# Kernel optimization log

Hardware: AMD Instinct MI355X
Metric: run time of the kernel (lower is better)

The kernel has to match this reference:

```python
import jax, jax.numpy as jnp
import numpy as np

N_NODES = 50000
N_EDGES = 800000
D_IN = 128
D_OUT = 128


def setup_inputs() -> dict:
    key = jax.random.key(0)
    k1, k2, k3, k4, k5, k6 = jax.random.split(key, 6)
    x = jax.random.normal(k1, (N_NODES, D_IN), dtype=jnp.float32)
    weight = jax.random.normal(k2, (D_IN, D_OUT), dtype=jnp.float32)
    bias = jax.random.normal(k3, (D_OUT,), dtype=jnp.float32)
    adj_row = jax.random.randint(k4, (N_EDGES,), 0, N_NODES, dtype=jnp.int64)
    adj_col = jax.random.randint(k5, (N_EDGES,), 0, N_NODES, dtype=jnp.int64)
    adj_val = jax.random.uniform(k6, (N_EDGES,), dtype=jnp.float32)
    return {"x": x, "weight": weight, "bias": bias,
            "adj_row": adj_row, "adj_col": adj_col, "adj_val": adj_val}


def reference(x, weight, bias, adj_row, adj_col, adj_val):
    # support = x @ W  -- dense GEMM [N, D_in] x [D_in, D_out]
    support = jnp.matmul(x, weight)
    # spmm(adj, support): out[i] = sum_e adj_val[e] * support[adj_col[e]] for adj_row[e]==i
    messages = support[adj_col] * adj_val[:, None]          # [E, D_out]
    output = jax.ops.segment_sum(messages, adj_row, num_segments=x.shape[0])
    return output + bias
```

## Files before the change

kernel.cpp:

```cpp
#include <hip/hip_runtime.h>

#define D 128
#define RPB 64
#define RPB_SHIFT 6
#define EPT 8
#define CHUNK (256 * EPT)
#define PASS_EDGES 1280

typedef __attribute__((ext_vector_type(8))) short short8;
typedef __attribute__((ext_vector_type(4))) float floatx4;
typedef __attribute__((ext_vector_type(4))) float f32x4;
typedef __attribute__((ext_vector_type(2))) unsigned int u32x2;
typedef unsigned int uint;
typedef unsigned short ushort;

__device__ inline short f2bf(float f) {
  unsigned u = __float_as_uint(f);
  u += 0x7FFF + ((u >> 16) & 1);
  return (short)(u >> 16);
}

__global__ __launch_bounds__(256) void gemm_hist_kernel(
    const float* __restrict__ x, const float* __restrict__ w,
    ushort* __restrict__ support, int n_nodes, int gemm_blocks,
    const int* __restrict__ adj_row, int* __restrict__ counts,
    int n_edges, int nb, int nc) {
  __shared__ short sWA[2 * 8 * 64 * 8];
  __shared__ int hist[1024];
  const int tid = threadIdx.x;

  if ((int)blockIdx.x < gemm_blocks) {
    const int wid = tid >> 6;
    const int lane = tid & 63;
    const int quad = lane >> 4;
    const int node = blockIdx.x * 64 + wid * 16 + (lane & 15);
    const bool ok = (node < n_nodes);

    floatx4 acc[8];
#pragma unroll
    for (int mt = 0; mt < 8; ++mt) acc[mt] = (floatx4){0.f, 0.f, 0.f, 0.f};

#pragma unroll
    for (int kt2 = 0; kt2 < 4; kt2 += 2) {
      if (kt2) __syncthreads();
      for (int s = tid; s < 1024; s += 256) {
        int ktmt = s >> 6, ls = s & 63;
        int kt = kt2 + (ktmt >> 3);
        int kb = kt * 32 + (ls >> 4) * 8;
        int m = (ktmt & 7) * 16 + (ls & 15);
        short8 frag;
#pragma unroll
        for (int j = 0; j < 8; ++j) frag[j] = f2bf(w[(kb + j) * D + m]);
        *(short8*)&sWA[s * 8] = frag;
      }
      __syncthreads();

#pragma unroll
      for (int ktoff = 0; ktoff < 2; ++ktoff) {
        const int kt = kt2 + ktoff;
        short8 bfr = (short8){0, 0, 0, 0, 0, 0, 0, 0};
        if (ok) {
          const float4 v0 = *(const float4*)&x[(size_t)node * D + kt * 32 + quad * 8];
          const float4 v1 = *(const float4*)&x[(size_t)node * D + kt * 32 + quad * 8 + 4];
          bfr = (short8){f2bf(v0.x), f2bf(v0.y), f2bf(v0.z), f2bf(v0.w),
                         f2bf(v1.x), f2bf(v1.y), f2bf(v1.z), f2bf(v1.w)};
        }
#pragma unroll
        for (int mt = 0; mt < 8; ++mt) {
          short8 a = *(const short8*)&sWA[((ktoff * 8 + mt) * 64 + lane) * 8];
          acc[mt] = __builtin_amdgcn_mfma_f32_16x16x32_bf16(a, bfr, acc[mt], 0, 0, 0);
        }
      }
    }

    if (ok) {
#pragma unroll
      for (int mt = 0; mt < 8; ++mt) {
        uint lo = ((uint)(ushort)f2bf(acc[mt][1]) << 16) | (ushort)f2bf(acc[mt][0]);
        uint hi = ((uint)(ushort)f2bf(acc[mt][3]) << 16) | (ushort)f2bf(acc[mt][2]);
        *(uint2*)&support[(size_t)node * D + mt * 16 + quad * 4] = make_uint2(lo, hi);
      }
    }
  } else {
    const int c = blockIdx.x - gemm_blocks;
    for (int i = tid; i < nb; i += 256) hist[i] = 0;
    __syncthreads();
    const int base = c * CHUNK + tid * EPT;
    if (base + EPT <= n_edges) {
      int4 r0 = *(const int4*)&adj_row[base];
      int4 r1 = *(const int4*)&adj_row[base + 4];
      int rr[EPT] = {r0.x, r0.y, r0.z, r0.w, r1.x, r1.y, r1.z, r1.w};
#pragma unroll
      for (int u = 0; u < EPT; ++u) atomicAdd(&hist[rr[u] >> RPB_SHIFT], 1);
    } else {
      for (int u = 0; u < EPT; ++u) {
        int e = base + u;
        if (e < n_edges) atomicAdd(&hist[adj_row[e] >> RPB_SHIFT], 1);
      }
    }
    __syncthreads();
    for (int b = tid; b < nb; b += 256)
      counts[(size_t)b * nc + c] = hist[b];
  }
}

__global__ __launch_bounds__(256) void scan_chunks_kernel(int* __restrict__ counts,
                                                          int* __restrict__ tot,
                                                          int nb, int nc) {
  __shared__ int buf[512];
  const int b = blockIdx.x;
  const int t = threadIdx.x;
  int v0 = (t < nc) ? counts[(size_t)b * nc + t] : 0;
  int v1 = (256 + t < nc) ? counts[(size_t)b * nc + 256 + t] : 0;
  buf[t] = v0;
  buf[256 + t] = v1;
  __syncthreads();
  for (int off = 1; off < 512; off <<= 1) {
    int a0 = buf[t], a1 = buf[256 + t];
    int d0 = (t >= off) ? buf[t - off] : 0;
    int d1 = (256 + t >= off) ? buf[256 + t - off] : 0;
    __syncthreads();
    buf[t] = a0 + d0;
    buf[256 + t] = a1 + d1;
    __syncthreads();
  }
  if (t < nc) counts[(size_t)b * nc + t] = buf[t] - v0;
  if (256 + t < nc) counts[(size_t)b * nc + 256 + t] = buf[256 + t] - v1;
  if (t == 0) tot[b] = buf[511];
}

__global__ __launch_bounds__(256) void scan_bins_kernel(const int* __restrict__ tot,
                                                        int* __restrict__ binStart,
                                                        int nb) {
  __shared__ int buf[1024];
  const int t = threadIdx.x;
  for (int i = t; i < 1024; i += 256) buf[i] = (i < nb) ? tot[i] : 0;
  __syncthreads();
  for (int off = 1; off < 1024; off <<= 1) {
    int a[4], d[4];
#pragma unroll
    for (int k = 0; k < 4; ++k) {
      int i = t + 256 * k;
      a[k] = buf[i];
      d[k] = (i >= off) ? buf[i - off] : 0;
    }
    __syncthreads();
#pragma unroll
    for (int k = 0; k < 4; ++k) buf[t + 256 * k] = a[k] + d[k];
    __syncthreads();
  }
  for (int i = t; i < nb; i += 256) binStart[i] = buf[i] - tot[i];
  if (t == 0) binStart[nb] = buf[1023];
}

__global__ __launch_bounds__(256) void sort_scatter_kernel(
    const int* __restrict__ adj_row, const int* __restrict__ adj_col,
    const float* __restrict__ adj_val, const int* __restrict__ rel,
    const int* __restrict__ binStart, uint2* __restrict__ sorted,
    int n_edges, int nb, int nc) {
  __shared__ int loff[1024];
  const int c = blockIdx.x;
  const int t = threadIdx.x;
  for (int i = t; i < nb; i += 256)
    loff[i] = binStart[i] + rel[(size_t)i * nc + c];
  __syncthreads();

  const int base = c * CHUNK + t * EPT;
  if (base + EPT <= n_edges) {
    int4 r0 = *(const int4*)&adj_row[base];
    int4 r1 = *(const int4*)&adj_row[base + 4];
    int4 c0 = *(const int4*)&adj_col[base];
    int4 c1 = *(const int4*)&adj_col[base + 4];
    float4 v0 = *(const float4*)&adj_val[base];
    float4 v1 = *(const float4*)&adj_val[base + 4];
    int rr[EPT] = {r0.x, r0.y, r0.z, r0.w, r1.x, r1.y, r1.z, r1.w};
    int cc[EPT] = {c0.x, c0.y, c0.z, c0.w, c1.x, c1.y, c1.z, c1.w};
    float vv[EPT] = {v0.x, v0.y, v0.z, v0.w, v1.x, v1.y, v1.z, v1.w};
#pragma unroll
    for (int u = 0; u < EPT; ++u) {
      int r = rr[u];
      int pos = atomicAdd(&loff[r >> RPB_SHIFT], 1);
      sorted[pos] = make_uint2(((uint)(r & (RPB - 1)) << 16) | (uint)cc[u],
                               __float_as_uint(vv[u]));
    }
  } else {
    for (int u = 0; u < EPT; ++u) {
      int e = base + u;
      if (e >= n_edges) break;
      int r = adj_row[e];
      int pos = atomicAdd(&loff[r >> RPB_SHIFT], 1);
      sorted[pos] = make_uint2(((uint)(r & (RPB - 1)) << 16) | (uint)adj_col[e],
                               __float_as_uint(adj_val[e]));
    }
  }
}

#define FMA8(vv, sv, IT)                                                  \
  do {                                                                    \
    acc[IT][0] = fmaf(vv, __uint_as_float((sv).x << 16), acc[IT][0]);     \
    acc[IT][1] = fmaf(vv, __uint_as_float((sv).x & 0xffff0000u), acc[IT][1]); \
    acc[IT][2] = fmaf(vv, __uint_as_float((sv).y << 16), acc[IT][2]);     \
    acc[IT][3] = fmaf(vv, __uint_as_float((sv).y & 0xffff0000u), acc[IT][3]); \
    acc[IT][4] = fmaf(vv, __uint_as_float((sv).z << 16), acc[IT][4]);     \
    acc[IT][5] = fmaf(vv, __uint_as_float((sv).z & 0xffff0000u), acc[IT][5]); \
    acc[IT][6] = fmaf(vv, __uint_as_float((sv).w << 16), acc[IT][6]);     \
    acc[IT][7] = fmaf(vv, __uint_as_float((sv).w & 0xffff0000u), acc[IT][7]); \
  } while (0)

__global__ __launch_bounds__(256) void bin_spmm_kernel(
    const uint2* __restrict__ sorted, const int* __restrict__ binStart,
    const uint* __restrict__ sup, const float* __restrict__ bias,
    float* __restrict__ out, int n_nodes) {
  __shared__ uint2 ebuf[PASS_EDGES];
  __shared__ int rowStart[RPB + 1];
  __shared__ int cursor[RPB];
  const int b = blockIdx.x;
  const int t = threadIdx.x;
  const int wid = t >> 6;
  const int lane = t & 63;
  const int qtr = lane >> 4;
  const int hl = lane & 15;

  const int s0 = binStart[b], s1 = binStart[b + 1];

  float acc[4][8];
#pragma unroll
  for (int it = 0; it < 4; ++it)
#pragma unroll
    for (int k = 0; k < 8; ++k) acc[it][k] = 0.f;

  for (int p0 = s0; p0 < s1; p0 += PASS_EDGES) {
    const int cntp = min(PASS_EDGES, s1 - p0);
    __syncthreads();
    if (t < RPB) cursor[t] = 0;
    __syncthreads();

    u32x2 er[8];
    int rr[8];
    const int base = p0 + t * EPT;
#pragma unroll
    for (int u = 0; u < EPT; ++u) {
      if (t * EPT + u < cntp) {
        er[u] = __builtin_nontemporal_load(
            (const u32x2*)&sorted[base + u]);
        rr[u] = (int)(er[u][0] >> 16);
        atomicAdd(&cursor[rr[u]], 1);
      } else {
        er[u] = (u32x2){0u, 0u};
        rr[u] = -1;
      }
    }
    __syncthreads();

    if (wid == 0) {
      int v = cursor[lane];
      int inc = v;
#pragma unroll
      for (int off = 1; off < 64; off <<= 1) {
        int u = __shfl_up(inc, off);
        if (lane >= off) inc += u;
      }
      rowStart[lane] = inc - v;
      if (lane == 63) rowStart[RPB] = inc;
    }
    __syncthreads();
    if (t < RPB) cursor[t] = rowStart[t];
    __syncthreads();

#pragma unroll
    for (int u = 0; u < EPT; ++u) {
      if (rr[u] >= 0) {
        int pos = atomicAdd(&cursor[rr[u]], 1);
        ebuf[pos] = make_uint2(er[u][0] & 0xFFFFu, er[u][1]);
      }
    }
    __syncthreads();

#pragma unroll
    for (int it = 0; it < 4; ++it) {
      const int rid = it * 16 + wid * 4 + qtr;
      const int js = rowStart[rid], je = rowStart[rid + 1];
      int j = js;
      for (; j + 8 <= je; j += 8) {
        uint cols[8];
        float vs[8];
#pragma unroll
        for (int u = 0; u < 8; ++u) {
          uint2 e = ebuf[j + u];
          cols[u] = e.x;
          vs[u] = __uint_as_float(e.y);
        }
        uint4 sv[8];
#pragma unroll
        for (int u = 0; u < 8; ++u)
          sv[u] = *(const uint4*)&sup[(size_t)cols[u] * 64 + hl * 4];
#pragma unroll
        for (int u = 0; u < 8; ++u) FMA8(vs[u], sv[u], it);
      }
      for (; j + 4 <= je; j += 4) {
        uint cols[4];
        float vs[4];
#pragma unroll
        for (int u = 0; u < 4; ++u) {
          uint2 e = ebuf[j + u];
          cols[u] = e.x;
          vs[u] = __uint_as_float(e.y);
        }
        uint4 sv[4];
#pragma unroll
        for (int u = 0; u < 4; ++u)
          sv[u] = *(const uint4*)&sup[(size_t)cols[u] * 64 + hl * 4];
#pragma unroll
        for (int u = 0; u < 4; ++u) FMA8(vs[u], sv[u], it);
      }
      for (; j < je; ++j) {
        uint2 e = ebuf[j];
        uint4 sv = *(const uint4*)&sup[(size_t)e.x * 64 + hl * 4];
        float v = __uint_as_float(e.y);
        FMA8(v, sv, it);
      }
    }
  }

  float4 b0 = *(const float4*)&bias[hl * 8];
  float4 b1 = *(const float4*)&bias[hl * 8 + 4];
#pragma unroll
  for (int it = 0; it < 4; ++it) {
    const int rid = it * 16 + wid * 4 + qtr;
    const int row = b * RPB + rid;
    if (row < n_nodes) {
      f32x4 o0 = {acc[it][0] + b0.x, acc[it][1] + b0.y,
                  acc[it][2] + b0.z, acc[it][3] + b0.w};
      f32x4 o1 = {acc[it][4] + b1.x, acc[it][5] + b1.y,
                  acc[it][6] + b1.z, acc[it][7] + b1.w};
      __builtin_nontemporal_store(o0, (f32x4*)&out[(size_t)row * D + hl * 8]);
      __builtin_nontemporal_store(o1, (f32x4*)&out[(size_t)row * D + hl * 8 + 4]);
    }
  }
}

extern "C" void kernel_launch(void* const* d_in, const int* in_sizes, int n_in,
                              void* d_out, int out_size, void* d_ws, size_t ws_size,
                              hipStream_t stream) {
  const float* x       = (const float*)d_in[0];
  const float* w       = (const float*)d_in[1];
  const float* bias    = (const float*)d_in[2];
  const int*   adj_row = (const int*)d_in[3];
  const int*   adj_col = (const int*)d_in[4];
  const float* adj_val = (const float*)d_in[5];

  const int n_nodes = in_sizes[0] / D;
  const int n_edges = in_sizes[3];
  float* out = (float*)d_out;

  const int nb = (n_nodes + RPB - 1) / RPB;
  const int nc = (n_edges + CHUNK - 1) / CHUNK;
  const int gemm_blocks = (n_nodes + 63) / 64;

  char* ws = (char*)d_ws;
  ushort* support  = (ushort*)ws; ws += ((size_t)n_nodes * D * 2 + 15) & ~15ull;
  int*    counts   = (int*)ws;    ws += ((size_t)nb * nc * 4 + 15) & ~15ull;
  int*    tot      = (int*)ws;    ws += ((size_t)nb * 4 + 15) & ~15ull;
  int*    binStart = (int*)ws;    ws += ((size_t)(nb + 1) * 4 + 15) & ~15ull;
  uint2*  sorted   = (uint2*)ws;  ws += (size_t)n_edges * 8;

  gemm_hist_kernel<<<gemm_blocks + nc, 256, 0, stream>>>(
      x, w, support, n_nodes, gemm_blocks, adj_row, counts, n_edges, nb, nc);

  scan_chunks_kernel<<<nb, 256, 0, stream>>>(counts, tot, nb, nc);

  scan_bins_kernel<<<1, 256, 0, stream>>>(tot, binStart, nb);

  sort_scatter_kernel<<<nc, 256, 0, stream>>>(adj_row, adj_col, adj_val,
                                              counts, binStart, sorted,
                                              n_edges, nb, nc);

  bin_spmm_kernel<<<nb, 256, 0, stream>>>(sorted, binStart, (const uint*)support,
                                          bias, out, n_nodes);
}
```

Before: 144.8 us.

## Pre-convert weights once and co-schedule GEMM with edge scatter kernel

Moves the fp32→bf16 transpose of the weight matrix into a small prologue alongside the histogram kernel, so each GEMM block loads ready bf16 fragments instead of redoing the strided conversion. The GEMM is moved from the histogram launch into the sort-scatter launch, so the short histogram kernel no longer waits on GEMM and the GEMM overlaps with the scatter. This adds a workspace buffer for the converted weights and makes the scatter blocks share a launch (and LDS sizing) with the GEMM blocks.

```diff
diff --git a/kernel.cpp b/kernel.cpp
--- a/kernel.cpp
+++ b/kernel.cpp
@@ -20,69 +20,15 @@
   return (short)(u >> 16);
 }
 
-__global__ __launch_bounds__(256) void gemm_hist_kernel(
-    const float* __restrict__ x, const float* __restrict__ w,
-    ushort* __restrict__ support, int n_nodes, int gemm_blocks,
+__global__ __launch_bounds__(256) void hist_wconv_kernel(
     const int* __restrict__ adj_row, int* __restrict__ counts,
-    int n_edges, int nb, int nc) {
-  __shared__ short sWA[2 * 8 * 64 * 8];
+    int n_edges, int nb, int nc,
+    const float* __restrict__ w, ushort* __restrict__ wt) {
   __shared__ int hist[1024];
   const int tid = threadIdx.x;
 
-  if ((int)blockIdx.x < gemm_blocks) {
-    const int wid = tid >> 6;
-    const int lane = tid & 63;
-    const int quad = lane >> 4;
-    const int node = blockIdx.x * 64 + wid * 16 + (lane & 15);
-    const bool ok = (node < n_nodes);
-
-    floatx4 acc[8];
-#pragma unroll
-    for (int mt = 0; mt < 8; ++mt) acc[mt] = (floatx4){0.f, 0.f, 0.f, 0.f};
-
-#pragma unroll
-    for (int kt2 = 0; kt2 < 4; kt2 += 2) {
-      if (kt2) __syncthreads();
-      for (int s = tid; s < 1024; s += 256) {
-        int ktmt = s >> 6, ls = s & 63;
-        int kt = kt2 + (ktmt >> 3);
-        int kb = kt * 32 + (ls >> 4) * 8;
-        int m = (ktmt & 7) * 16 + (ls & 15);
-        short8 frag;
-#pragma unroll
-        for (int j = 0; j < 8; ++j) frag[j] = f2bf(w[(kb + j) * D + m]);
-        *(short8*)&sWA[s * 8] = frag;
-      }
-      __syncthreads();
-
-#pragma unroll
-      for (int ktoff = 0; ktoff < 2; ++ktoff) {
-        const int kt = kt2 + ktoff;
-        short8 bfr = (short8){0, 0, 0, 0, 0, 0, 0, 0};
-        if (ok) {
-          const float4 v0 = *(const float4*)&x[(size_t)node * D + kt * 32 + quad * 8];
-          const float4 v1 = *(const float4*)&x[(size_t)node * D + kt * 32 + quad * 8 + 4];
-          bfr = (short8){f2bf(v0.x), f2bf(v0.y), f2bf(v0.z), f2bf(v0.w),
-                         f2bf(v1.x), f2bf(v1.y), f2bf(v1.z), f2bf(v1.w)};
-        }
-#pragma unroll
-        for (int mt = 0; mt < 8; ++mt) {
-          short8 a = *(const short8*)&sWA[((ktoff * 8 + mt) * 64 + lane) * 8];
-          acc[mt] = __builtin_amdgcn_mfma_f32_16x16x32_bf16(a, bfr, acc[mt], 0, 0, 0);
-        }
-      }
-    }
-
-    if (ok) {
-#pragma unroll
-      for (int mt = 0; mt < 8; ++mt) {
-        uint lo = ((uint)(ushort)f2bf(acc[mt][1]) << 16) | (ushort)f2bf(acc[mt][0]);
-        uint hi = ((uint)(ushort)f2bf(acc[mt][3]) << 16) | (ushort)f2bf(acc[mt][2]);
-        *(uint2*)&support[(size_t)node * D + mt * 16 + quad * 4] = make_uint2(lo, hi);
-      }
-    }
-  } else {
-    const int c = blockIdx.x - gemm_blocks;
+  if ((int)blockIdx.x < nc) {
+    const int c = blockIdx.x;
     for (int i = tid; i < nb; i += 256) hist[i] = 0;
     __syncthreads();
     const int base = c * CHUNK + tid * EPT;
@@ -101,6 +47,14 @@
     __syncthreads();
     for (int b = tid; b < nb; b += 256)
       counts[(size_t)b * nc + c] = hist[b];
+  } else {
+    const int idx = ((int)blockIdx.x - nc) * 256 + tid;
+    const int m = idx >> 4;
+    const int ks = (idx & 15) * 8;
+    short8 frag;
+#pragma unroll
+    for (int j = 0; j < 8; ++j) frag[j] = f2bf(w[(ks + j) * D + m]);
+    *(short8*)&wt[(size_t)m * D + ks] = frag;
   }
 }
 
@@ -153,44 +107,99 @@
   if (t == 0) binStart[nb] = buf[1023];
 }
 
-__global__ __launch_bounds__(256) void sort_scatter_kernel(
+__global__ __launch_bounds__(256) void gemm_sort_kernel(
+    const float* __restrict__ x, const ushort* __restrict__ wt,
+    ushort* __restrict__ support, int n_nodes, int gemm_blocks,
     const int* __restrict__ adj_row, const int* __restrict__ adj_col,
     const float* __restrict__ adj_val, const int* __restrict__ rel,
     const int* __restrict__ binStart, uint2* __restrict__ sorted,
     int n_edges, int nb, int nc) {
-  __shared__ int loff[1024];
-  const int c = blockIdx.x;
-  const int t = threadIdx.x;
-  for (int i = t; i < nb; i += 256)
-    loff[i] = binStart[i] + rel[(size_t)i * nc + c];
-  __syncthreads();
-
-  const int base = c * CHUNK + t * EPT;
-  if (base + EPT <= n_edges) {
-    int4 r0 = *(const int4*)&adj_row[base];
-    int4 r1 = *(const int4*)&adj_row[base + 4];
-    int4 c0 = *(const int4*)&adj_col[base];
-    int4 c1 = *(const int4*)&adj_col[base + 4];
-    float4 v0 = *(const float4*)&adj_val[base];
-    float4 v1 = *(const float4*)&adj_val[base + 4];
-    int rr[EPT] = {r0.x, r0.y, r0.z, r0.w, r1.x, r1.y, r1.z, r1.w};
-    int cc[EPT] = {c0.x, c0.y, c0.z, c0.w, c1.x, c1.y, c1.z, c1.w};
-    float vv[EPT] = {v0.x, v0.y, v0.z, v0.w, v1.x, v1.y, v1.z, v1.w};
-#pragma unroll
-    for (int u = 0; u < EPT; ++u) {
-      int r = rr[u];
-      int pos = atomicAdd(&loff[r >> RPB_SHIFT], 1);
-      sorted[pos] = make_uint2(((uint)(r & (RPB - 1)) << 16) | (uint)cc[u],
-                               __float_as_uint(vv[u]));
+  __shared__ short sWA[2 * 8 * 64 * 8];
+  const int tid = threadIdx.x;
+
+  if ((int)blockIdx.x < gemm_blocks) {
+    const int wid = tid >> 6;
+    const int lane = tid & 63;
+    const int quad = lane >> 4;
+    const int node = blockIdx.x * 64 + wid * 16 + (lane & 15);
+    const bool ok = (node < n_nodes);
+
+    floatx4 acc[8];
+#pragma unroll
+    for (int mt = 0; mt < 8; ++mt) acc[mt] = (floatx4){0.f, 0.f, 0.f, 0.f};
+
+#pragma unroll
+    for (int kt2 = 0; kt2 < 4; kt2 += 2) {
+      if (kt2) __syncthreads();
+      for (int s = tid; s < 1024; s += 256) {
+        int ktmt = s >> 6, ls = s & 63;
+        int kt = kt2 + (ktmt >> 3);
+        int kb = kt * 32 + (ls >> 4) * 8;
+        int m = (ktmt & 7) * 16 + (ls & 15);
+        *(short8*)&sWA[s * 8] = *(const short8*)&wt[(size_t)m * D + kb];
+      }
+      __syncthreads();
+
+#pragma unroll
+      for (int ktoff = 0; ktoff < 2; ++ktoff) {
+        const int kt = kt2 + ktoff;
+        short8 bfr = (short8){0, 0, 0, 0, 0, 0, 0, 0};
+        if (ok) {
+          const float4 v0 = *(const float4*)&x[(size_t)node * D + kt * 32 + quad * 8];
+          const float4 v1 = *(const float4*)&x[(size_t)node * D + kt * 32 + quad * 8 + 4];
+          bfr = (short8){f2bf(v0.x), f2bf(v0.y), f2bf(v0.z), f2bf(v0.w),
+                         f2bf(v1.x), f2bf(v1.y), f2bf(v1.z), f2bf(v1.w)};
+        }
+#pragma unroll
+        for (int mt = 0; mt < 8; ++mt) {
+          short8 a = *(const short8*)&sWA[((ktoff * 8 + mt) * 64 + lane) * 8];
+          acc[mt] = __builtin_amdgcn_mfma_f32_16x16x32_bf16(a, bfr, acc[mt], 0, 0, 0);
+        }
+      }
+    }
+
+    if (ok) {
+#pragma unroll
+      for (int mt = 0; mt < 8; ++mt) {
+        uint lo = ((uint)(ushort)f2bf(acc[mt][1]) << 16) | (ushort)f2bf(acc[mt][0]);
+        uint hi = ((uint)(ushort)f2bf(acc[mt][3]) << 16) | (ushort)f2bf(acc[mt][2]);
+        *(uint2*)&support[(size_t)node * D + mt * 16 + quad * 4] = make_uint2(lo, hi);
+      }
     }
   } else {
-    for (int u = 0; u < EPT; ++u) {
-      int e = base + u;
-      if (e >= n_edges) break;
-      int r = adj_row[e];
-      int pos = atomicAdd(&loff[r >> RPB_SHIFT], 1);
-      sorted[pos] = make_uint2(((uint)(r & (RPB - 1)) << 16) | (uint)adj_col[e],
-                               __float_as_uint(adj_val[e]));
+    int* loff = (int*)sWA;
+    const int c = (int)blockIdx.x - gemm_blocks;
+    for (int i = tid; i < nb; i += 256)
+      loff[i] = binStart[i] + rel[(size_t)i * nc + c];
+    __syncthreads();
+
+    const int base = c * CHUNK + tid * EPT;
+    if (base + EPT <= n_edges) {
+      int4 r0 = *(const int4*)&adj_row[base];
+      int4 r1 = *(const int4*)&adj_row[base + 4];
+      int4 c0 = *(const int4*)&adj_col[base];
+      int4 c1 = *(const int4*)&adj_col[base + 4];
+      float4 v0 = *(const float4*)&adj_val[base];
+      float4 v1 = *(const float4*)&adj_val[base + 4];
+      int rr[EPT] = {r0.x, r0.y, r0.z, r0.w, r1.x, r1.y, r1.z, r1.w};
+      int cc[EPT] = {c0.x, c0.y, c0.z, c0.w, c1.x, c1.y, c1.z, c1.w};
+      float vv[EPT] = {v0.x, v0.y, v0.z, v0.w, v1.x, v1.y, v1.z, v1.w};
+#pragma unroll
+      for (int u = 0; u < EPT; ++u) {
+        int r = rr[u];
+        int pos = atomicAdd(&loff[r >> RPB_SHIFT], 1);
+        sorted[pos] = make_uint2(((uint)(r & (RPB - 1)) << 16) | (uint)cc[u],
+                                 __float_as_uint(vv[u]));
+      }
+    } else {
+      for (int u = 0; u < EPT; ++u) {
+        int e = base + u;
+        if (e >= n_edges) break;
+        int r = adj_row[e];
+        int pos = atomicAdd(&loff[r >> RPB_SHIFT], 1);
+        sorted[pos] = make_uint2(((uint)(r & (RPB - 1)) << 16) | (uint)adj_col[e],
+                                 __float_as_uint(adj_val[e]));
+      }
     }
   }
 }
@@ -362,18 +371,19 @@
   int*    counts   = (int*)ws;    ws += ((size_t)nb * nc * 4 + 15) & ~15ull;
   int*    tot      = (int*)ws;    ws += ((size_t)nb * 4 + 15) & ~15ull;
   int*    binStart = (int*)ws;    ws += ((size_t)(nb + 1) * 4 + 15) & ~15ull;
+  ushort* wt       = (ushort*)ws; ws += (size_t)D * D * 2;
   uint2*  sorted   = (uint2*)ws;  ws += (size_t)n_edges * 8;
 
-  gemm_hist_kernel<<<gemm_blocks + nc, 256, 0, stream>>>(
-      x, w, support, n_nodes, gemm_blocks, adj_row, counts, n_edges, nb, nc);
+  hist_wconv_kernel<<<nc + 8, 256, 0, stream>>>(adj_row, counts, n_edges, nb, nc,
+                                                w, wt);
 
   scan_chunks_kernel<<<nb, 256, 0, stream>>>(counts, tot, nb, nc);
 
   scan_bins_kernel<<<1, 256, 0, stream>>>(tot, binStart, nb);
 
-  sort_scatter_kernel<<<nc, 256, 0, stream>>>(adj_row, adj_col, adj_val,
-                                              counts, binStart, sorted,
-                                              n_edges, nb, nc);
+  gemm_sort_kernel<<<gemm_blocks + nc, 256, 0, stream>>>(
+      x, wt, support, n_nodes, gemm_blocks,
+      adj_row, adj_col, adj_val, counts, binStart, sorted, n_edges, nb, nc);
 
   bin_spmm_kernel<<<nb, 256, 0, stream>>>(sorted, binStart, (const uint*)support,
                                           bias, out, n_nodes);
```

New measurement: 142.4 us. Within noise of the previous version (-1.7%).
